# Performance work log

Hardware: AMD Instinct MI355X
Metric: run time of the kernel (lower is better)

Reference implementation:

```python
import jax, jax.numpy as jnp
import numpy as np

D_QKV = 64

def setup_inputs() -> dict:
    key = jax.random.key(0)
    k1, k2, k3, k4 = jax.random.split(key, 4)
    B, T, D = 4, 2048, 1024
    x = jax.random.normal(k1, (B, T, D), dtype=jnp.float32)
    Wq = jax.random.normal(k2, (D, D_QKV), dtype=jnp.float32) * (D ** -0.5)
    Wk = jax.random.normal(k3, (D, D_QKV), dtype=jnp.float32) * (D ** -0.5)
    Wv = jax.random.normal(k4, (D, D_QKV), dtype=jnp.float32) * (D ** -0.5)
    return {"x": x, "Wq": Wq, "Wk": Wk, "Wv": Wv}

def reference(x, Wq, Wk, Wv):
    # x: [B, T, D]; single-head causal attention with head dim d_qkv
    T = x.shape[1]
    q = jnp.einsum("btd,de->bte", x, Wq)  # [B, T, d]
    k = jnp.einsum("btd,de->bte", x, Wk)
    v = jnp.einsum("btd,de->bte", x, Wv)
    scores = jnp.einsum("bqe,bke->bqk", q, k) / (D_QKV ** 0.5)  # [B, T, T]
    causal = jnp.tril(jnp.ones((T, T), dtype=bool))
    scores = jnp.where(causal, scores, -jnp.inf)
    attn = jax.nn.softmax(scores, axis=2)
    return jnp.einsum("bqk,bke->bqe", attn, v)  # [B, T, d]
```

## Files before the change

kernel.cpp:

```cpp
#include <hip/hip_runtime.h>
#include <hip/hip_bf16.h>

typedef __hip_bfloat16 bf16;
typedef __bf16 bf16x8 __attribute__((ext_vector_type(8)));
typedef float f32x4 __attribute__((ext_vector_type(4)));
typedef unsigned short u16x8 __attribute__((ext_vector_type(8)));

#define B_SZ   4
#define T_SEQ  2048
#define D_IN   1024
#define D_QKV  64
#define BT     (B_SZ * T_SEQ)
#define PSTR   72

#define GLD_LDS(gp, lp) __builtin_amdgcn_global_load_lds(                     \
    (const __attribute__((address_space(1))) void*)(gp),                      \
    (__attribute__((address_space(3))) void*)(lp), 16, 0, 0)

__global__ __launch_bounds__(256) void wt_prep(
    const float* __restrict__ Wq, const float* __restrict__ Wk,
    const float* __restrict__ Wv, bf16* __restrict__ wt)
{
    __shared__ float ws[64 * 65];
    const int bx = blockIdx.x;
    const int m  = bx >> 4;
    const int k0 = (bx & 15) << 6;
    const float* W = (m == 0) ? Wq : (m == 1) ? Wk : Wv;
    const int tid = threadIdx.x;
    #pragma unroll
    for (int i = 0; i < 16; ++i) {
        const int idx = i * 256 + tid;
        const int kk = idx >> 6, nn = idx & 63;
        ws[kk * 65 + nn] = W[(size_t)(k0 + kk) * D_QKV + nn];
    }
    __syncthreads();
    const int n = tid >> 2, kq = (tid & 3) << 4;
    bf16 tmp[16];
    #pragma unroll
    for (int j = 0; j < 16; ++j)
        tmp[j] = __float2bfloat16(ws[(kq + j) * 65 + n]);
    uint4* dst = (uint4*)(wt + (size_t)(m * 64 + n) * D_IN + k0 + kq);
    dst[0] = ((uint4*)tmp)[0];
    dst[1] = ((uint4*)tmp)[1];
}

__global__ __launch_bounds__(256) void qkv_proj_mfma(
    const float* __restrict__ x, const bf16* __restrict__ wt,
    bf16* __restrict__ qb, bf16* __restrict__ kb, bf16* __restrict__ vt)
{
    __shared__ uint4 As[2][1024];
    __shared__ uint4 Bs[2][768];

    const int tid  = threadIdx.x;
    const int wave = tid >> 6;
    const int lane = tid & 63;
    const int col  = lane & 15;
    const int quad = lane >> 4;
    const int bx   = blockIdx.x;
    const int m0   = (bx >> 1) * 64;
    const int ng   = bx & 1;

    f32x4 acc[6];
    #pragma unroll
    for (int i = 0; i < 6; ++i) acc[i] = (f32x4){0.f, 0.f, 0.f, 0.f};

    auto stage = [&](int it, int buf) {
        const int k0 = it * 64;
        #pragma unroll
        for (int j = 0; j < 7; ++j) {
            const int s = wave + j * 4;
            if (s < 16) {
                const int c = s * 64 + lane;
                const int r = c >> 4;
                const int ccl = ((c & 15) - r) & 15;
                const float* g = x + (size_t)(m0 + r) * D_IN + k0 + ccl * 4;
                GLD_LDS(g, &As[buf][s * 64]);
            } else {
                const int bs = s - 16;
                const int c = bs * 64 + lane;
                const int n = c >> 3;
                const int ccl = ((c & 7) - n) & 7;
                const bf16* g = wt + (size_t)(ng * 96 + n) * D_IN + k0 + ccl * 8;
                GLD_LDS(g, &Bs[buf][bs * 64]);
            }
        }
    };

    stage(0, 0);
    const int r = wave * 16 + col;
    #pragma unroll 1
    for (int it = 0; it < 16; ++it) {
        __syncthreads();
        if (it + 1 < 16) stage(it + 1, (it + 1) & 1);
        const float4* Ac = (const float4*)As[it & 1];
        const uint4*  Bc = Bs[it & 1];
        #pragma unroll
        for (int s = 0; s < 2; ++s) {
            const int ca = s * 8 + quad * 2;
            const float4 a0 = Ac[r * 16 + ((ca + r) & 15)];
            const float4 a1 = Ac[r * 16 + ((ca + 1 + r) & 15)];
            const bf16x8 af = (bf16x8){(__bf16)a0.x, (__bf16)a0.y, (__bf16)a0.z, (__bf16)a0.w,
                                       (__bf16)a1.x, (__bf16)a1.y, (__bf16)a1.z, (__bf16)a1.w};
            #pragma unroll
            for (int i = 0; i < 6; ++i) {
                const int n = i * 16 + col;
                const bf16x8 bfr = __builtin_bit_cast(bf16x8,
                    Bc[n * 8 + ((s * 4 + quad + n) & 7)]);
                acc[i] = __builtin_amdgcn_mfma_f32_16x16x32_bf16(af, bfr, acc[i], 0, 0, 0);
            }
        }
    }

    const int bb = m0 >> 11;
    const int tl = m0 & (T_SEQ - 1);
    #pragma unroll
    for (int i = 0; i < 6; ++i) {
        const int n = ng * 96 + i * 16 + col;
        #pragma unroll
        for (int rr = 0; rr < 4; ++rr) {
            const int row = m0 + wave * 16 + quad * 4 + rr;
            const bf16 vq = __float2bfloat16(acc[i][rr]);
            if (n < 64)       qb[(size_t)row * D_QKV + n] = vq;
            else if (n < 128) kb[(size_t)row * D_QKV + (n - 64)] = vq;
            else              vt[(size_t)bb * D_QKV * T_SEQ + (size_t)(n - 128) * T_SEQ
                                 + (tl + wave * 16 + quad * 4 + rr)] = vq;
        }
    }
}

__global__ __launch_bounds__(256) void attn_kernel(
    const bf16* __restrict__ qb, const bf16* __restrict__ kb,
    const bf16* __restrict__ vt, float* __restrict__ Op, float* __restrict__ lp)
{
    __shared__ uint4 Ks[2][512];
    __shared__ uint4 Vs[2][512];
    __shared__ unsigned short plds[4 * 16 * PSTR];

    const int tid  = threadIdx.x;
    const int wave = tid >> 6;
    const int lane = tid & 63;
    const int col  = lane & 15;
    const int quad = lane >> 4;
    const int bx   = blockIdx.x;
    const int tile    = (bx < 256) ? (127 - (bx >> 2)) : ((bx - 256) >> 2);
    const int quarter = bx & 3;
    const int b    = tile >> 5;
    const int qloc = (tile & 31) * 64;
    const int nch  = (tile & 31) + 1;

    const bf16* kbp = kb + (size_t)b * T_SEQ * D_QKV;
    const bf16* vtp = vt + (size_t)b * D_QKV * T_SEQ;
    const uint4* q4 = (const uint4*)(qb + (size_t)b * T_SEQ * D_QKV);

    const bf16x8 aq0 = __builtin_bit_cast(bf16x8, q4[(qloc + wave * 16 + col) * 8 + quad]);
    const bf16x8 aq1 = __builtin_bit_cast(bf16x8, q4[(qloc + wave * 16 + col) * 8 + 4 + quad]);

    f32x4 o[4];
    float ls[4];
    #pragma unroll
    for (int dt = 0; dt < 4; ++dt) o[dt] = (f32x4){0.f, 0.f, 0.f, 0.f};
    #pragma unroll
    for (int rr = 0; rr < 4; ++rr) ls[rr] = 0.f;

    unsigned short* pl = plds + wave * 16 * PSTR;
    const u16x8* p8 = (const u16x8*)pl;

    auto stage = [&](int c, int buf) {
        const int kb0 = c * 64;
        #pragma unroll
        for (int j = 0; j < 4; ++j) {
            const int s = wave + j * 4;
            if (s < 8) {
                const int ch = s * 64 + lane;
                const int key = ch >> 3;
                const int ccl = ((ch & 7) - key) & 7;
                const bf16* g = kbp + (size_t)(kb0 + key) * D_QKV + ccl * 8;
                GLD_LDS(g, &Ks[buf][s * 64]);
            } else {
                const int vs = s - 8;
                const int ch = vs * 64 + lane;
                const int d = ch >> 3;
                const int ccl = ((ch & 7) - d) & 7;
                const bf16* g = vtp + (size_t)d * T_SEQ + kb0 + ccl * 8;
                GLD_LDS(g, &Vs[buf][vs * 64]);
            }
        }
    };

    if (quarter < nch) stage(quarter, 0);
    int i = 0;
    for (int c = quarter; c < nch; c += 4, ++i) {
        __syncthreads();
        if (c + 4 < nch) stage(c + 4, (i + 1) & 1);
        const uint4* Kc = Ks[i & 1];
        const uint4* Vc = Vs[i & 1];

        f32x4 sc[4];
        #pragma unroll
        for (int nt = 0; nt < 4; ++nt) {
            const int kp = nt * 16 + col;
            const bf16x8 bk0 = __builtin_bit_cast(bf16x8, Kc[kp * 8 + ((quad + kp) & 7)]);
            const bf16x8 bk1 = __builtin_bit_cast(bf16x8, Kc[kp * 8 + ((4 + quad + kp) & 7)]);
            sc[nt] = (f32x4){0.f, 0.f, 0.f, 0.f};
            sc[nt] = __builtin_amdgcn_mfma_f32_16x16x32_bf16(aq0, bk0, sc[nt], 0, 0, 0);
            sc[nt] = __builtin_amdgcn_mfma_f32_16x16x32_bf16(aq1, bk1, sc[nt], 0, 0, 0);
        }

        if (c == nch - 1) {
            #pragma unroll
            for (int nt = 0; nt < 4; ++nt) {
                const int kp = c * 64 + nt * 16 + col;
                #pragma unroll
                for (int rr = 0; rr < 4; ++rr)
                    if (kp > qloc + wave * 16 + quad * 4 + rr) sc[nt][rr] = -INFINITY;
            }
        }

        #pragma unroll
        for (int nt = 0; nt < 4; ++nt) {
            #pragma unroll
            for (int rr = 0; rr < 4; ++rr) {
                const float pv = __expf(sc[nt][rr] * 0.125f);
                ls[rr] += pv;
                pl[(quad * 4 + rr) * PSTR + nt * 16 + col] =
                    __builtin_bit_cast(unsigned short, __float2bfloat16(pv));
            }
        }

        const bf16x8 pa0 = __builtin_bit_cast(bf16x8, p8[col * 9 + quad]);
        const bf16x8 pa1 = __builtin_bit_cast(bf16x8, p8[col * 9 + 4 + quad]);

        #pragma unroll
        for (int dt = 0; dt < 4; ++dt) {
            const int dp = dt * 16 + col;
            const bf16x8 bv0 = __builtin_bit_cast(bf16x8, Vc[dp * 8 + ((quad + dp) & 7)]);
            const bf16x8 bv1 = __builtin_bit_cast(bf16x8, Vc[dp * 8 + ((4 + quad + dp) & 7)]);
            o[dt] = __builtin_amdgcn_mfma_f32_16x16x32_bf16(pa0, bv0, o[dt], 0, 0, 0);
            o[dt] = __builtin_amdgcn_mfma_f32_16x16x32_bf16(pa1, bv1, o[dt], 0, 0, 0);
        }
    }

    #pragma unroll
    for (int rr = 0; rr < 4; ++rr) {
        #pragma unroll
        for (int msk = 1; msk < 16; msk <<= 1)
            ls[rr] += __shfl_xor(ls[rr], msk);
    }

    const int pbase = (tile * 4 + quarter) * 64 + wave * 16;
    #pragma unroll
    for (int dt = 0; dt < 4; ++dt)
        #pragma unroll
        for (int rr = 0; rr < 4; ++rr)
            Op[(size_t)(pbase + quad * 4 + rr) * D_QKV + dt * 16 + col] = o[dt][rr];
    if (col == 0) {
        #pragma unroll
        for (int rr = 0; rr < 4; ++rr)
            lp[pbase + quad * 4 + rr] = ls[rr];
    }
}

__global__ __launch_bounds__(256) void combine_attn(
    const float* __restrict__ Op, const float* __restrict__ lp,
    float* __restrict__ out)
{
    const int idx = blockIdx.x * 256 + threadIdx.x;
    const int qg = idx >> 6, d = idx & 63;
    const int tile = qg >> 6, qq = qg & 63;
    float s = 0.f, l = 0.f;
    #pragma unroll
    for (int k = 0; k < 4; ++k) {
        s += Op[(size_t)((tile * 4 + k) * 64 + qq) * D_QKV + d];
        l += lp[(tile * 4 + k) * 64 + qq];
    }
    out[(size_t)qg * D_QKV + d] = s / l;
}

extern "C" void kernel_launch(void* const* d_in, const int* in_sizes, int n_in,
                              void* d_out, int out_size, void* d_ws, size_t ws_size,
                              hipStream_t stream) {
    const float* x  = (const float*)d_in[0];
    const float* Wq = (const float*)d_in[1];
    const float* Wk = (const float*)d_in[2];
    const float* Wv = (const float*)d_in[3];
    float* out = (float*)d_out;

    char* ws = (char*)d_ws;
    bf16*  qb = (bf16*)(ws);
    bf16*  kb = (bf16*)(ws + (1u << 20));
    bf16*  vt = (bf16*)(ws + (2u << 20));
    bf16*  wt = (bf16*)(ws + (3u << 20));
    float* Op = (float*)(ws + (4u << 20));
    float* lp = (float*)(ws + (12u << 20));

    wt_prep<<<48, 256, 0, stream>>>(Wq, Wk, Wv, wt);
    qkv_proj_mfma<<<256, 256, 0, stream>>>(x, wt, qb, kb, vt);
    attn_kernel<<<512, 256, 0, stream>>>(qb, kb, vt, Op, lp);
    combine_attn<<<2048, 256, 0, stream>>>(Op, lp, out);
}
```

Baseline: 109.8 us.

## Fuse all four kernels into one persistent kernel with grid barriers

Merges weight prep, QKV projection, attention and the combine step into a single 512-block launch separated by software grid barriers built on global atomic counters. The projection is retiled to 32-row blocks so 512 blocks cover it, and the cross-quarter combine now runs in whichever block finishes a tile last, tracked by a per-tile atomic counter. This removes three kernel launches and the inter-kernel gaps, at the cost of spin-wait barriers that rely on all 512 blocks being co-resident. The counters are never reset: the grid barrier rounds its target up to the next multiple of 512, and the tile counter relies on its count modulo 4.

```diff
diff --git a/kernel.cpp b/kernel.cpp
--- a/kernel.cpp
+++ b/kernel.cpp
@@ -12,44 +12,39 @@
 #define D_QKV  64
 #define BT     (B_SZ * T_SEQ)
 #define PSTR   72
+#define NBLK   512
 
 #define GLD_LDS(gp, lp) __builtin_amdgcn_global_load_lds(                     \
     (const __attribute__((address_space(1))) void*)(gp),                      \
     (__attribute__((address_space(3))) void*)(lp), 16, 0, 0)
 
-__global__ __launch_bounds__(256) void wt_prep(
-    const float* __restrict__ Wq, const float* __restrict__ Wk,
-    const float* __restrict__ Wv, bf16* __restrict__ wt)
-{
-    __shared__ float ws[64 * 65];
-    const int bx = blockIdx.x;
-    const int m  = bx >> 4;
-    const int k0 = (bx & 15) << 6;
-    const float* W = (m == 0) ? Wq : (m == 1) ? Wk : Wv;
-    const int tid = threadIdx.x;
-    #pragma unroll
-    for (int i = 0; i < 16; ++i) {
-        const int idx = i * 256 + tid;
-        const int kk = idx >> 6, nn = idx & 63;
-        ws[kk * 65 + nn] = W[(size_t)(k0 + kk) * D_QKV + nn];
+__device__ int g_bar1 = 0;
+__device__ int g_bar2 = 0;
+__device__ int g_tile[128] = {};
+
+__device__ __forceinline__ void grid_barrier(int* ctr) {
+    __syncthreads();
+    if (threadIdx.x == 0) {
+        __threadfence();
+        const int old = atomicAdd(ctr, 1);
+        const int tgt = (old & ~(NBLK - 1)) + NBLK;
+        while (__hip_atomic_load(ctr, __ATOMIC_RELAXED,
+                                 __HIP_MEMORY_SCOPE_AGENT) < tgt)
+            __builtin_amdgcn_s_sleep(2);
+        __threadfence();
     }
     __syncthreads();
-    const int n = tid >> 2, kq = (tid & 3) << 4;
-    bf16 tmp[16];
-    #pragma unroll
-    for (int j = 0; j < 16; ++j)
-        tmp[j] = __float2bfloat16(ws[(kq + j) * 65 + n]);
-    uint4* dst = (uint4*)(wt + (size_t)(m * 64 + n) * D_IN + k0 + kq);
-    dst[0] = ((uint4*)tmp)[0];
-    dst[1] = ((uint4*)tmp)[1];
 }
 
-__global__ __launch_bounds__(256) void qkv_proj_mfma(
-    const float* __restrict__ x, const bf16* __restrict__ wt,
-    bf16* __restrict__ qb, bf16* __restrict__ kb, bf16* __restrict__ vt)
+__global__ __launch_bounds__(256, 2) void fused_attn(
+    const float* __restrict__ x,  const float* __restrict__ Wq,
+    const float* __restrict__ Wk, const float* __restrict__ Wv,
+    bf16* __restrict__ wt, bf16* __restrict__ qb, bf16* __restrict__ kb,
+    bf16* __restrict__ vt, float* __restrict__ Op, float* __restrict__ lp,
+    float* __restrict__ out)
 {
-    __shared__ uint4 As[2][1024];
-    __shared__ uint4 Bs[2][768];
+    __shared__ __align__(16) char smem[41984];
+    __shared__ int lastf;
 
     const int tid  = threadIdx.x;
     const int wave = tid >> 6;
@@ -57,223 +52,251 @@
     const int col  = lane & 15;
     const int quad = lane >> 4;
     const int bx   = blockIdx.x;
-    const int m0   = (bx >> 1) * 64;
-    const int ng   = bx & 1;
-
-    f32x4 acc[6];
-    #pragma unroll
-    for (int i = 0; i < 6; ++i) acc[i] = (f32x4){0.f, 0.f, 0.f, 0.f};
-
-    auto stage = [&](int it, int buf) {
-        const int k0 = it * 64;
-        #pragma unroll
-        for (int j = 0; j < 7; ++j) {
-            const int s = wave + j * 4;
-            if (s < 16) {
-                const int c = s * 64 + lane;
-                const int r = c >> 4;
-                const int ccl = ((c & 15) - r) & 15;
-                const float* g = x + (size_t)(m0 + r) * D_IN + k0 + ccl * 4;
-                GLD_LDS(g, &As[buf][s * 64]);
-            } else {
-                const int bs = s - 16;
-                const int c = bs * 64 + lane;
-                const int n = c >> 3;
-                const int ccl = ((c & 7) - n) & 7;
-                const bf16* g = wt + (size_t)(ng * 96 + n) * D_IN + k0 + ccl * 8;
-                GLD_LDS(g, &Bs[buf][bs * 64]);
-            }
-        }
-    };
-
-    stage(0, 0);
-    const int r = wave * 16 + col;
-    #pragma unroll 1
-    for (int it = 0; it < 16; ++it) {
+
+    if (bx < 48) {
+        float* wsT = (float*)smem;
+        const int m  = bx >> 4;
+        const int k0 = (bx & 15) << 6;
+        const float* W = (m == 0) ? Wq : (m == 1) ? Wk : Wv;
+        #pragma unroll
+        for (int i = 0; i < 16; ++i) {
+            const int idx = i * 256 + tid;
+            const int kk = idx >> 6, nn = idx & 63;
+            wsT[kk * 65 + nn] = W[(size_t)(k0 + kk) * D_QKV + nn];
+        }
         __syncthreads();
-        if (it + 1 < 16) stage(it + 1, (it + 1) & 1);
-        const float4* Ac = (const float4*)As[it & 1];
-        const uint4*  Bc = Bs[it & 1];
-        #pragma unroll
-        for (int s = 0; s < 2; ++s) {
-            const int ca = s * 8 + quad * 2;
-            const float4 a0 = Ac[r * 16 + ((ca + r) & 15)];
-            const float4 a1 = Ac[r * 16 + ((ca + 1 + r) & 15)];
-            const bf16x8 af = (bf16x8){(__bf16)a0.x, (__bf16)a0.y, (__bf16)a0.z, (__bf16)a0.w,
-                                       (__bf16)a1.x, (__bf16)a1.y, (__bf16)a1.z, (__bf16)a1.w};
-            #pragma unroll
-            for (int i = 0; i < 6; ++i) {
-                const int n = i * 16 + col;
-                const bf16x8 bfr = __builtin_bit_cast(bf16x8,
-                    Bc[n * 8 + ((s * 4 + quad + n) & 7)]);
-                acc[i] = __builtin_amdgcn_mfma_f32_16x16x32_bf16(af, bfr, acc[i], 0, 0, 0);
-            }
-        }
+        const int n = tid >> 2, kq = (tid & 3) << 4;
+        bf16 tmp[16];
+        #pragma unroll
+        for (int j = 0; j < 16; ++j)
+            tmp[j] = __float2bfloat16(wsT[(kq + j) * 65 + n]);
+        uint4* dst = (uint4*)(wt + (size_t)(m * 64 + n) * D_IN + k0 + kq);
+        dst[0] = ((uint4*)tmp)[0];
+        dst[1] = ((uint4*)tmp)[1];
     }
-
-    const int bb = m0 >> 11;
-    const int tl = m0 & (T_SEQ - 1);
-    #pragma unroll
-    for (int i = 0; i < 6; ++i) {
-        const int n = ng * 96 + i * 16 + col;
+    grid_barrier(&g_bar1);
+
+    {
+        uint4 (*As)[512] = reinterpret_cast<uint4(*)[512]>(smem);
+        uint4 (*Bs)[768] = reinterpret_cast<uint4(*)[768]>(smem + 16384);
+        const int m0 = (bx >> 1) * 32;
+        const int ng = bx & 1;
+
+        f32x4 acc[3];
+        #pragma unroll
+        for (int i = 0; i < 3; ++i) acc[i] = (f32x4){0.f, 0.f, 0.f, 0.f};
+
+        auto stage = [&](int it, int buf) {
+            const int k0 = it * 64;
+            #pragma unroll
+            for (int j = 0; j < 5; ++j) {
+                const int s = wave + j * 4;
+                if (s < 8) {
+                    const int c = s * 64 + lane;
+                    const int r = c >> 4;
+                    const int ccl = ((c & 15) - r) & 15;
+                    const float* g = x + (size_t)(m0 + r) * D_IN + k0 + ccl * 4;
+                    GLD_LDS(g, &As[buf][s * 64]);
+                } else {
+                    const int bs = s - 8;
+                    const int c = bs * 64 + lane;
+                    const int n = c >> 3;
+                    const int ccl = ((c & 7) - n) & 7;
+                    const bf16* g = wt + (size_t)(ng * 96 + n) * D_IN + k0 + ccl * 8;
+                    GLD_LDS(g, &Bs[buf][bs * 64]);
+                }
+            }
+        };
+
+        stage(0, 0);
+        const int r  = (wave >> 1) * 16 + col;
+        const int nh = wave & 1;
+        #pragma unroll 1
+        for (int it = 0; it < 16; ++it) {
+            __syncthreads();
+            if (it + 1 < 16) stage(it + 1, (it + 1) & 1);
+            const float4* Ac = (const float4*)As[it & 1];
+            const uint4*  Bc = Bs[it & 1];
+            #pragma unroll
+            for (int s = 0; s < 2; ++s) {
+                const int ca = s * 8 + quad * 2;
+                const float4 a0 = Ac[r * 16 + ((ca + r) & 15)];
+                const float4 a1 = Ac[r * 16 + ((ca + 1 + r) & 15)];
+                const bf16x8 af = (bf16x8){(__bf16)a0.x, (__bf16)a0.y, (__bf16)a0.z, (__bf16)a0.w,
+                                           (__bf16)a1.x, (__bf16)a1.y, (__bf16)a1.z, (__bf16)a1.w};
+                #pragma unroll
+                for (int i = 0; i < 3; ++i) {
+                    const int n = nh * 48 + i * 16 + col;
+                    const bf16x8 bfr = __builtin_bit_cast(bf16x8,
+                        Bc[n * 8 + ((s * 4 + quad + n) & 7)]);
+                    acc[i] = __builtin_amdgcn_mfma_f32_16x16x32_bf16(af, bfr, acc[i], 0, 0, 0);
+                }
+            }
+        }
+
+        const int bb = m0 >> 11;
+        const int tl = m0 & (T_SEQ - 1);
+        #pragma unroll
+        for (int i = 0; i < 3; ++i) {
+            const int n = ng * 96 + nh * 48 + i * 16 + col;
+            #pragma unroll
+            for (int rr = 0; rr < 4; ++rr) {
+                const int row = m0 + (wave >> 1) * 16 + quad * 4 + rr;
+                const bf16 vq = __float2bfloat16(acc[i][rr]);
+                if (n < 64)       qb[(size_t)row * D_QKV + n] = vq;
+                else if (n < 128) kb[(size_t)row * D_QKV + (n - 64)] = vq;
+                else              vt[(size_t)bb * D_QKV * T_SEQ + (size_t)(n - 128) * T_SEQ
+                                     + (tl + (wave >> 1) * 16 + quad * 4 + rr)] = vq;
+            }
+        }
+    }
+    grid_barrier(&g_bar2);
+
+    {
+        uint4 (*Ks)[512] = reinterpret_cast<uint4(*)[512]>(smem);
+        uint4 (*Vs)[512] = reinterpret_cast<uint4(*)[512]>(smem + 16384);
+        unsigned short* plds = (unsigned short*)(smem + 32768);
+
+        const int tile    = (bx < 256) ? (127 - (bx >> 2)) : ((bx - 256) >> 2);
+        const int quarter = bx & 3;
+        const int b    = tile >> 5;
+        const int qloc = (tile & 31) * 64;
+        const int nch  = (tile & 31) + 1;
+
+        const bf16* kbp = kb + (size_t)b * T_SEQ * D_QKV;
+        const bf16* vtp = vt + (size_t)b * D_QKV * T_SEQ;
+        const uint4* q4 = (const uint4*)(qb + (size_t)b * T_SEQ * D_QKV);
+
+        const bf16x8 aq0 = __builtin_bit_cast(bf16x8, q4[(qloc + wave * 16 + col) * 8 + quad]);
+        const bf16x8 aq1 = __builtin_bit_cast(bf16x8, q4[(qloc + wave * 16 + col) * 8 + 4 + quad]);
+
+        f32x4 o[4];
+        float ls[4];
+        #pragma unroll
+        for (int dt = 0; dt < 4; ++dt) o[dt] = (f32x4){0.f, 0.f, 0.f, 0.f};
+        #pragma unroll
+        for (int rr = 0; rr < 4; ++rr) ls[rr] = 0.f;
+
+        unsigned short* pl = plds + wave * 16 * PSTR;
+        const u16x8* p8 = (const u16x8*)pl;
+
+        auto stage = [&](int c, int buf) {
+            const int kb0 = c * 64;
+            #pragma unroll
+            for (int j = 0; j < 4; ++j) {
+                const int s = wave + j * 4;
+                if (s < 8) {
+                    const int ch = s * 64 + lane;
+                    const int key = ch >> 3;
+                    const int ccl = ((ch & 7) - key) & 7;
+                    const bf16* g = kbp + (size_t)(kb0 + key) * D_QKV + ccl * 8;
+                    GLD_LDS(g, &Ks[buf][s * 64]);
+                } else {
+                    const int vs = s - 8;
+                    const int ch = vs * 64 + lane;
+                    const int d = ch >> 3;
+                    const int ccl = ((ch & 7) - d) & 7;
+                    const bf16* g = vtp + (size_t)d * T_SEQ + kb0 + ccl * 8;
+                    GLD_LDS(g, &Vs[buf][vs * 64]);
+                }
+            }
+        };
+
+        if (quarter < nch) stage(quarter, 0);
+        int i = 0;
+        for (int c = quarter; c < nch; c += 4, ++i) {
+            __syncthreads();
+            if (c + 4 < nch) stage(c + 4, (i + 1) & 1);
+            const uint4* Kc = Ks[i & 1];
+            const uint4* Vc = Vs[i & 1];
+
+            f32x4 sc[4];
+            #pragma unroll
+            for (int nt = 0; nt < 4; ++nt) {
+                const int kp = nt * 16 + col;
+                const bf16x8 bk0 = __builtin_bit_cast(bf16x8, Kc[kp * 8 + ((quad + kp) & 7)]);
+                const bf16x8 bk1 = __builtin_bit_cast(bf16x8, Kc[kp * 8 + ((4 + quad + kp) & 7)]);
+                sc[nt] = (f32x4){0.f, 0.f, 0.f, 0.f};
+                sc[nt] = __builtin_amdgcn_mfma_f32_16x16x32_bf16(aq0, bk0, sc[nt], 0, 0, 0);
+                sc[nt] = __builtin_amdgcn_mfma_f32_16x16x32_bf16(aq1, bk1, sc[nt], 0, 0, 0);
+            }
+
+            if (c == nch - 1) {
+                #pragma unroll
+                for (int nt = 0; nt < 4; ++nt) {
+                    const int kp = c * 64 + nt * 16 + col;
+                    #pragma unroll
+                    for (int rr = 0; rr < 4; ++rr)
+                        if (kp > qloc + wave * 16 + quad * 4 + rr) sc[nt][rr] = -INFINITY;
+                }
+            }
+
+            #pragma unroll
+            for (int nt = 0; nt < 4; ++nt) {
+                #pragma unroll
+                for (int rr = 0; rr < 4; ++rr) {
+                    const float pv = __expf(sc[nt][rr] * 0.125f);
+                    ls[rr] += pv;
+                    pl[(quad * 4 + rr) * PSTR + nt * 16 + col] =
+                        __builtin_bit_cast(unsigned short, __float2bfloat16(pv));
+                }
+            }
+
+            const bf16x8 pa0 = __builtin_bit_cast(bf16x8, p8[col * 9 + quad]);
+            const bf16x8 pa1 = __builtin_bit_cast(bf16x8, p8[col * 9 + 4 + quad]);
+
+            #pragma unroll
+            for (int dt = 0; dt < 4; ++dt) {
+                const int dp = dt * 16 + col;
+                const bf16x8 bv0 = __builtin_bit_cast(bf16x8, Vc[dp * 8 + ((quad + dp) & 7)]);
+                const bf16x8 bv1 = __builtin_bit_cast(bf16x8, Vc[dp * 8 + ((4 + quad + dp) & 7)]);
+                o[dt] = __builtin_amdgcn_mfma_f32_16x16x32_bf16(pa0, bv0, o[dt], 0, 0, 0);
+                o[dt] = __builtin_amdgcn_mfma_f32_16x16x32_bf16(pa1, bv1, o[dt], 0, 0, 0);
+            }
+        }
+
         #pragma unroll
         for (int rr = 0; rr < 4; ++rr) {
-            const int row = m0 + wave * 16 + quad * 4 + rr;
-            const bf16 vq = __float2bfloat16(acc[i][rr]);
-            if (n < 64)       qb[(size_t)row * D_QKV + n] = vq;
-            else if (n < 128) kb[(size_t)row * D_QKV + (n - 64)] = vq;
-            else              vt[(size_t)bb * D_QKV * T_SEQ + (size_t)(n - 128) * T_SEQ
-                                 + (tl + wave * 16 + quad * 4 + rr)] = vq;
+            #pragma unroll
+            for (int msk = 1; msk < 16; msk <<= 1)
+                ls[rr] += __shfl_xor(ls[rr], msk);
+        }
+
+        const int pbase = (tile * 4 + quarter) * 64 + wave * 16;
+        #pragma unroll
+        for (int dt = 0; dt < 4; ++dt)
+            #pragma unroll
+            for (int rr = 0; rr < 4; ++rr)
+                Op[(size_t)(pbase + quad * 4 + rr) * D_QKV + dt * 16 + col] = o[dt][rr];
+        if (col == 0) {
+            #pragma unroll
+            for (int rr = 0; rr < 4; ++rr)
+                lp[pbase + quad * 4 + rr] = ls[rr];
+        }
+
+        __threadfence();
+        __syncthreads();
+        if (tid == 0) lastf = ((atomicAdd(&g_tile[tile], 1) & 3) == 3);
+        __syncthreads();
+        if (lastf) {
+            __threadfence();
+            #pragma unroll
+            for (int t4 = tid; t4 < 1024; t4 += 256) {
+                const int qq = t4 >> 4, d4 = (t4 & 15) << 2;
+                float4 s = {0.f, 0.f, 0.f, 0.f};
+                float l = 0.f;
+                #pragma unroll
+                for (int k = 0; k < 4; ++k) {
+                    const float4 p = *(const float4*)&Op[(size_t)((tile * 4 + k) * 64 + qq) * D_QKV + d4];
+                    s.x += p.x; s.y += p.y; s.z += p.z; s.w += p.w;
+                    l += lp[(tile * 4 + k) * 64 + qq];
+                }
+                const float rl = 1.f / l;
+                const float4 o4 = {s.x * rl, s.y * rl, s.z * rl, s.w * rl};
+                *(float4*)&out[(size_t)(tile * 64 + qq) * D_QKV + d4] = o4;
+            }
         }
     }
-}
-
-__global__ __launch_bounds__(256) void attn_kernel(
-    const bf16* __restrict__ qb, const bf16* __restrict__ kb,
-    const bf16* __restrict__ vt, float* __restrict__ Op, float* __restrict__ lp)
-{
-    __shared__ uint4 Ks[2][512];
-    __shared__ uint4 Vs[2][512];
-    __shared__ unsigned short plds[4 * 16 * PSTR];
-
-    const int tid  = threadIdx.x;
-    const int wave = tid >> 6;
-    const int lane = tid & 63;
-    const int col  = lane & 15;
-    const int quad = lane >> 4;
-    const int bx   = blockIdx.x;
-    const int tile    = (bx < 256) ? (127 - (bx >> 2)) : ((bx - 256) >> 2);
-    const int quarter = bx & 3;
-    const int b    = tile >> 5;
-    const int qloc = (tile & 31) * 64;
-    const int nch  = (tile & 31) + 1;
-
-    const bf16* kbp = kb + (size_t)b * T_SEQ * D_QKV;
-    const bf16* vtp = vt + (size_t)b * D_QKV * T_SEQ;
-    const uint4* q4 = (const uint4*)(qb + (size_t)b * T_SEQ * D_QKV);
-
-    const bf16x8 aq0 = __builtin_bit_cast(bf16x8, q4[(qloc + wave * 16 + col) * 8 + quad]);
-    const bf16x8 aq1 = __builtin_bit_cast(bf16x8, q4[(qloc + wave * 16 + col) * 8 + 4 + quad]);
-
-    f32x4 o[4];
-    float ls[4];
-    #pragma unroll
-    for (int dt = 0; dt < 4; ++dt) o[dt] = (f32x4){0.f, 0.f, 0.f, 0.f};
-    #pragma unroll
-    for (int rr = 0; rr < 4; ++rr) ls[rr] = 0.f;
-
-    unsigned short* pl = plds + wave * 16 * PSTR;
-    const u16x8* p8 = (const u16x8*)pl;
-
-    auto stage = [&](int c, int buf) {
-        const int kb0 = c * 64;
-        #pragma unroll
-        for (int j = 0; j < 4; ++j) {
-            const int s = wave + j * 4;
-            if (s < 8) {
-                const int ch = s * 64 + lane;
-                const int key = ch >> 3;
-                const int ccl = ((ch & 7) - key) & 7;
-                const bf16* g = kbp + (size_t)(kb0 + key) * D_QKV + ccl * 8;
-                GLD_LDS(g, &Ks[buf][s * 64]);
-            } else {
-                const int vs = s - 8;
-                const int ch = vs * 64 + lane;
-                const int d = ch >> 3;
-                const int ccl = ((ch & 7) - d) & 7;
-                const bf16* g = vtp + (size_t)d * T_SEQ + kb0 + ccl * 8;
-                GLD_LDS(g, &Vs[buf][vs * 64]);
-            }
-        }
-    };
-
-    if (quarter < nch) stage(quarter, 0);
-    int i = 0;
-    for (int c = quarter; c < nch; c += 4, ++i) {
-        __syncthreads();
-        if (c + 4 < nch) stage(c + 4, (i + 1) & 1);
-        const uint4* Kc = Ks[i & 1];
-        const uint4* Vc = Vs[i & 1];
-
-        f32x4 sc[4];
-        #pragma unroll
-        for (int nt = 0; nt < 4; ++nt) {
-            const int kp = nt * 16 + col;
-            const bf16x8 bk0 = __builtin_bit_cast(bf16x8, Kc[kp * 8 + ((quad + kp) & 7)]);
-            const bf16x8 bk1 = __builtin_bit_cast(bf16x8, Kc[kp * 8 + ((4 + quad + kp) & 7)]);
-            sc[nt] = (f32x4){0.f, 0.f, 0.f, 0.f};
-            sc[nt] = __builtin_amdgcn_mfma_f32_16x16x32_bf16(aq0, bk0, sc[nt], 0, 0, 0);
-            sc[nt] = __builtin_amdgcn_mfma_f32_16x16x32_bf16(aq1, bk1, sc[nt], 0, 0, 0);
-        }
-
-        if (c == nch - 1) {
-            #pragma unroll
-            for (int nt = 0; nt < 4; ++nt) {
-                const int kp = c * 64 + nt * 16 + col;
-                #pragma unroll
-                for (int rr = 0; rr < 4; ++rr)
-                    if (kp > qloc + wave * 16 + quad * 4 + rr) sc[nt][rr] = -INFINITY;
-            }
-        }
-
-        #pragma unroll
-        for (int nt = 0; nt < 4; ++nt) {
-            #pragma unroll
-            for (int rr = 0; rr < 4; ++rr) {
-                const float pv = __expf(sc[nt][rr] * 0.125f);
-                ls[rr] += pv;
-                pl[(quad * 4 + rr) * PSTR + nt * 16 + col] =
-                    __builtin_bit_cast(unsigned short, __float2bfloat16(pv));
-            }
-        }
-
-        const bf16x8 pa0 = __builtin_bit_cast(bf16x8, p8[col * 9 + quad]);
-        const bf16x8 pa1 = __builtin_bit_cast(bf16x8, p8[col * 9 + 4 + quad]);
-
-        #pragma unroll
-        for (int dt = 0; dt < 4; ++dt) {
-            const int dp = dt * 16 + col;
-            const bf16x8 bv0 = __builtin_bit_cast(bf16x8, Vc[dp * 8 + ((quad + dp) & 7)]);
-            const bf16x8 bv1 = __builtin_bit_cast(bf16x8, Vc[dp * 8 + ((4 + quad + dp) & 7)]);
-            o[dt] = __builtin_amdgcn_mfma_f32_16x16x32_bf16(pa0, bv0, o[dt], 0, 0, 0);
-            o[dt] = __builtin_amdgcn_mfma_f32_16x16x32_bf16(pa1, bv1, o[dt], 0, 0, 0);
-        }
-    }
-
-    #pragma unroll
-    for (int rr = 0; rr < 4; ++rr) {
-        #pragma unroll
-        for (int msk = 1; msk < 16; msk <<= 1)
-            ls[rr] += __shfl_xor(ls[rr], msk);
-    }
-
-    const int pbase = (tile * 4 + quarter) * 64 + wave * 16;
-    #pragma unroll
-    for (int dt = 0; dt < 4; ++dt)
-        #pragma unroll
-        for (int rr = 0; rr < 4; ++rr)
-            Op[(size_t)(pbase + quad * 4 + rr) * D_QKV + dt * 16 + col] = o[dt][rr];
-    if (col == 0) {
-        #pragma unroll
-        for (int rr = 0; rr < 4; ++rr)
-            lp[pbase + quad * 4 + rr] = ls[rr];
-    }
-}
-
-__global__ __launch_bounds__(256) void combine_attn(
-    const float* __restrict__ Op, const float* __restrict__ lp,
-    float* __restrict__ out)
-{
-    const int idx = blockIdx.x * 256 + threadIdx.x;
-    const int qg = idx >> 6, d = idx & 63;
-    const int tile = qg >> 6, qq = qg & 63;
-    float s = 0.f, l = 0.f;
-    #pragma unroll
-    for (int k = 0; k < 4; ++k) {
-        s += Op[(size_t)((tile * 4 + k) * 64 + qq) * D_QKV + d];
-        l += lp[(tile * 4 + k) * 64 + qq];
-    }
-    out[(size_t)qg * D_QKV + d] = s / l;
 }
 
 extern "C" void kernel_launch(void* const* d_in, const int* in_sizes, int n_in,
@@ -293,8 +316,5 @@
     float* Op = (float*)(ws + (4u << 20));
     float* lp = (float*)(ws + (12u << 20));
 
-    wt_prep<<<48, 256, 0, stream>>>(Wq, Wk, Wv, wt);
-    qkv_proj_mfma<<<256, 256, 0, stream>>>(x, wt, qb, kb, vt);
-    attn_kernel<<<512, 256, 0, stream>>>(qb, kb, vt, Op, lp);
-    combine_attn<<<2048, 256, 0, stream>>>(Op, lp, out);
+    fused_attn<<<NBLK, 256, 0, stream>>>(x, Wq, Wk, Wv, wt, qb, kb, vt, Op, lp, out);
 }
```

Result: slower. 290.4 us (+164.6%).
